# Kernel tuning notes

Hardware: AMD Instinct MI355X
Metric: run time of the kernel (lower is better)

The kernel has to match this reference:

```python
import jax, jax.numpy as jnp
import numpy as np

KNN = 4
H = 0.03


def setup_inputs() -> dict:
    key = jax.random.key(0)
    pc = jax.random.normal(key, (8, 4096, 3), dtype=jnp.float32)  # [B, N, 3]
    return {"pc": pc}


def reference(pc) -> jnp.ndarray:
    sq = jnp.sum(pc * pc, axis=-1)  # [B, N]
    # dist[b, i, j] = || pc[b,i] - pc[b,j] ||^2
    dist = sq[:, :, None] + sq[:, None, :] - 2.0 * jnp.einsum("bid,bjd->bij", pc, pc)
    dist = jnp.maximum(dist, 0.0)
    # k nearest neighbors with offset=1 (skip self): take smallest KNN+1, drop the first
    neg_top, _ = jax.lax.top_k(-dist, KNN + 1)  # sorted descending -> distances ascending
    knn_dist = -neg_top[..., 1:]  # [B, N, KNN]
    weight = jnp.exp(-knn_dist / (H * H))
    loss = jnp.sum(-knn_dist * weight)
    return loss
```

## Files before the change

### kernel.cpp

```cpp
#include <hip/hip_runtime.h>
#include <math.h>

#define NPTS   4096
#define NB     8
#define TILE   64
#define NWAVES 8
#define BLK    (NWAVES * 64)
#define JCHUNK (NPTS / NWAVES)
#define INV_H2 (1.0f / (0.03f * 0.03f))

__device__ __forceinline__ float med3f(float a, float b, float c) {
#if defined(__has_builtin)
#if __has_builtin(__builtin_amdgcn_fmed3f)
  return __builtin_amdgcn_fmed3f(a, b, c);
#else
  return fminf(c, fmaxf(a, b));
#endif
#else
  return fminf(c, fmaxf(a, b));
#endif
}

template <bool CHECK>
__device__ __forceinline__ void scan_range(const float4* __restrict__ sP,
                                           int lo, int hi, int self,
                                           float mx, float my, float mz, float sqi,
                                           float& t0, float& t1, float& t2, float& t3) {
#pragma unroll 8
  for (int j = lo; j < hi; ++j) {
    float4 q = sP[j];
    float t = fmaf(mz, q.z, q.w);
    t = fmaf(my, q.y, t);
    t = fmaf(mx, q.x, t);
    float d = t + sqi;
    if (CHECK) d = (j == self) ? 3.0e38f : d;
    t3 = med3f(t2, d, t3);
    t2 = med3f(t1, d, t2);
    t1 = med3f(t0, d, t1);
    t0 = fminf(t0, d);
  }
}

__device__ __forceinline__ void merge4(float a0, float a1, float a2, float a3,
                                       float b0, float b1, float b2, float b3,
                                       float& o0, float& o1, float& o2, float& o3) {
  float L0 = fminf(a0, b3), L1 = fminf(a1, b2), L2 = fminf(a2, b1), L3 = fminf(a3, b0);
  float e0 = fminf(L0, L2), e2 = fmaxf(L0, L2);
  float e1 = fminf(L1, L3), e3 = fmaxf(L1, L3);
  o0 = fminf(e0, e1); o1 = fmaxf(e0, e1);
  o2 = fminf(e2, e3); o3 = fmaxf(e2, e3);
}

__global__ __launch_bounds__(BLK)
void repulsion_kernel(const float* __restrict__ pc, float* __restrict__ out) {
  __shared__ float4 sP[NPTS];
  __shared__ float4 cand4[NWAVES * TILE];

  const int blk  = blockIdx.x;
  const int b    = blk >> 6;
  const int tile = blk & 63;
  const int tid  = threadIdx.x;
  const float* base = pc + (size_t)b * NPTS * 3;
  const float4* pcv = (const float4*)base;

  for (int g = tid; g < NPTS / 4; g += BLK) {
    float4 a = pcv[3 * g + 0];
    float4 c = pcv[3 * g + 1];
    float4 e = pcv[3 * g + 2];
    float x0 = a.x, y0 = a.y, z0 = a.z;
    float x1 = a.w, y1 = c.x, z1 = c.y;
    float x2 = c.z, y2 = c.w, z2 = e.x;
    float x3 = e.y, y3 = e.z, z3 = e.w;
    sP[4 * g + 0] = make_float4(x0, y0, z0, fmaf(x0, x0, fmaf(y0, y0, z0 * z0)));
    sP[4 * g + 1] = make_float4(x1, y1, z1, fmaf(x1, x1, fmaf(y1, y1, z1 * z1)));
    sP[4 * g + 2] = make_float4(x2, y2, z2, fmaf(x2, x2, fmaf(y2, y2, z2 * z2)));
    sP[4 * g + 3] = make_float4(x3, y3, z3, fmaf(x3, x3, fmaf(y3, y3, z3 * z3)));
  }
  __syncthreads();

  const int w    = tid >> 6;
  const int lane = tid & 63;
  const int self = tile * TILE + lane;

  float4 me = sP[self];
  const float mx = -2.0f * me.x, my = -2.0f * me.y, mz = -2.0f * me.z;
  const float sqi = me.w;

  const float INF = 3.0e38f;
  float t0 = INF, t1 = INF, t2 = INF, t3 = INF;

  const int j0 = w * JCHUNK;
  const int selfwave = tile >> 3;
  if (w == selfwave) {
    const int s0 = tile * TILE;
    scan_range<false>(sP, j0, s0, self, mx, my, mz, sqi, t0, t1, t2, t3);
    scan_range<true >(sP, s0, s0 + TILE, self, mx, my, mz, sqi, t0, t1, t2, t3);
    scan_range<false>(sP, s0 + TILE, j0 + JCHUNK, self, mx, my, mz, sqi, t0, t1, t2, t3);
  } else {
    scan_range<false>(sP, j0, j0 + JCHUNK, self, mx, my, mz, sqi, t0, t1, t2, t3);
  }

  cand4[w * TILE + lane] = make_float4(t0, t1, t2, t3);
  __syncthreads();

  if (tid < 64) {
    float4 A = cand4[0 * TILE + lane];
    float4 B = cand4[1 * TILE + lane];
    float4 C = cand4[2 * TILE + lane];
    float4 D = cand4[3 * TILE + lane];
    float4 E = cand4[4 * TILE + lane];
    float4 F = cand4[5 * TILE + lane];
    float4 G = cand4[6 * TILE + lane];
    float4 H4 = cand4[7 * TILE + lane];
    float ab0, ab1, ab2, ab3, cd0, cd1, cd2, cd3;
    float ef0, ef1, ef2, ef3, gh0, gh1, gh2, gh3;
    merge4(A.x, A.y, A.z, A.w, B.x, B.y, B.z, B.w, ab0, ab1, ab2, ab3);
    merge4(C.x, C.y, C.z, C.w, D.x, D.y, D.z, D.w, cd0, cd1, cd2, cd3);
    merge4(E.x, E.y, E.z, E.w, F.x, F.y, F.z, F.w, ef0, ef1, ef2, ef3);
    merge4(G.x, G.y, G.z, G.w, H4.x, H4.y, H4.z, H4.w, gh0, gh1, gh2, gh3);
    float u0, u1, u2, u3, v0, v1, v2, v3;
    merge4(ab0, ab1, ab2, ab3, cd0, cd1, cd2, cd3, u0, u1, u2, u3);
    merge4(ef0, ef1, ef2, ef3, gh0, gh1, gh2, gh3, v0, v1, v2, v3);
    float m0 = fminf(u0, v3);
    float m1 = fminf(u1, v2);
    float m2 = fminf(u2, v1);
    float m3 = fminf(u3, v0);

    float s = 0.0f;
    s -= m0 * expf(-m0 * INV_H2);
    s -= m1 * expf(-m1 * INV_H2);
    s -= m2 * expf(-m2 * INV_H2);
    s -= m3 * expf(-m3 * INV_H2);

    for (int off = 32; off > 0; off >>= 1) s += __shfl_down(s, off);
    if (lane == 0) atomicAdd(out, s);
  }
}

extern "C" void kernel_launch(void* const* d_in, const int* in_sizes, int n_in,
                              void* d_out, int out_size, void* d_ws, size_t ws_size,
                              hipStream_t stream) {
  const float* pc = (const float*)d_in[0];
  float* out = (float*)d_out;
  hipMemsetAsync(out, 0, sizeof(float), stream);
  repulsion_kernel<<<dim3(NB * (NPTS / TILE)), dim3(BLK), 0, stream>>>(pc, out);
}
```

Baseline: 82.17 us.

## Process two query points per thread and use 16 waves per block

Each thread now tracks top-4 lists for two query points, so every shared-memory load of a candidate point serves two distance computations. Blocks grow to 1024 threads (16 waves), each covering 128 query points, and the grid halves to 256 blocks. The final merge becomes a 16-way tree over 128 threads. This cuts LDS traffic per distance and the number of redundant per-block staging passes, at the cost of more registers, fewer blocks to fill the GPU, and a longer cross-wave merge.

```diff
diff --git a/kernel.cpp b/kernel.cpp
--- a/kernel.cpp
+++ b/kernel.cpp
@@ -3,11 +3,12 @@
 
 #define NPTS   4096
 #define NB     8
-#define TILE   64
-#define NWAVES 8
+#define IGRP   128
+#define NWAVES 16
 #define BLK    (NWAVES * 64)
 #define JCHUNK (NPTS / NWAVES)
 #define INV_H2 (1.0f / (0.03f * 0.03f))
+#define INFD   3.0e38f
 
 __device__ __forceinline__ float med3f(float a, float b, float c) {
 #if defined(__has_builtin)
@@ -22,109 +23,115 @@
 }
 
 template <bool CHECK>
-__device__ __forceinline__ void scan_range(const float4* __restrict__ sP,
-                                           int lo, int hi, int self,
-                                           float mx, float my, float mz, float sqi,
-                                           float& t0, float& t1, float& t2, float& t3) {
+__device__ __forceinline__ void scan_range(
+    const float4* __restrict__ sP, int lo, int hi, int i0, int i1,
+    float mx0, float my0, float mz0, float sq0,
+    float mx1, float my1, float mz1, float sq1,
+    float& a0, float& a1, float& a2, float& a3,
+    float& b0, float& b1, float& b2, float& b3) {
 #pragma unroll 8
   for (int j = lo; j < hi; ++j) {
     float4 q = sP[j];
-    float t = fmaf(mz, q.z, q.w);
-    t = fmaf(my, q.y, t);
-    t = fmaf(mx, q.x, t);
-    float d = t + sqi;
-    if (CHECK) d = (j == self) ? 3.0e38f : d;
-    t3 = med3f(t2, d, t3);
-    t2 = med3f(t1, d, t2);
-    t1 = med3f(t0, d, t1);
-    t0 = fminf(t0, d);
+    float u = fmaf(mz0, q.z, q.w);
+    u = fmaf(my0, q.y, u);
+    u = fmaf(mx0, q.x, u);
+    float d0 = u + sq0;
+    float v = fmaf(mz1, q.z, q.w);
+    v = fmaf(my1, q.y, v);
+    v = fmaf(mx1, q.x, v);
+    float d1 = v + sq1;
+    if (CHECK) {
+      d0 = (j == i0) ? INFD : d0;
+      d1 = (j == i1) ? INFD : d1;
+    }
+    a3 = med3f(a2, d0, a3); a2 = med3f(a1, d0, a2);
+    a1 = med3f(a0, d0, a1); a0 = fminf(a0, d0);
+    b3 = med3f(b2, d1, b3); b2 = med3f(b1, d1, b2);
+    b1 = med3f(b0, d1, b1); b0 = fminf(b0, d1);
   }
 }
 
-__device__ __forceinline__ void merge4(float a0, float a1, float a2, float a3,
-                                       float b0, float b1, float b2, float b3,
-                                       float& o0, float& o1, float& o2, float& o3) {
-  float L0 = fminf(a0, b3), L1 = fminf(a1, b2), L2 = fminf(a2, b1), L3 = fminf(a3, b0);
+__device__ __forceinline__ float4 merge4(float4 A, float4 B) {
+  float L0 = fminf(A.x, B.w), L1 = fminf(A.y, B.z);
+  float L2 = fminf(A.z, B.y), L3 = fminf(A.w, B.x);
   float e0 = fminf(L0, L2), e2 = fmaxf(L0, L2);
   float e1 = fminf(L1, L3), e3 = fmaxf(L1, L3);
-  o0 = fminf(e0, e1); o1 = fmaxf(e0, e1);
-  o2 = fminf(e2, e3); o3 = fmaxf(e2, e3);
+  return make_float4(fminf(e0, e1), fmaxf(e0, e1), fminf(e2, e3), fmaxf(e2, e3));
 }
 
 __global__ __launch_bounds__(BLK)
 void repulsion_kernel(const float* __restrict__ pc, float* __restrict__ out) {
   __shared__ float4 sP[NPTS];
-  __shared__ float4 cand4[NWAVES * TILE];
+  __shared__ float4 cand[NWAVES * IGRP];
 
   const int blk  = blockIdx.x;
-  const int b    = blk >> 6;
-  const int tile = blk & 63;
+  const int b    = blk >> 5;
+  const int g    = blk & 31;
   const int tid  = threadIdx.x;
-  const float* base = pc + (size_t)b * NPTS * 3;
-  const float4* pcv = (const float4*)base;
+  const float4* pcv = (const float4*)(pc + (size_t)b * NPTS * 3);
 
-  for (int g = tid; g < NPTS / 4; g += BLK) {
-    float4 a = pcv[3 * g + 0];
-    float4 c = pcv[3 * g + 1];
-    float4 e = pcv[3 * g + 2];
+  {
+    int k = tid;
+    float4 a = pcv[3 * k + 0];
+    float4 c = pcv[3 * k + 1];
+    float4 e = pcv[3 * k + 2];
     float x0 = a.x, y0 = a.y, z0 = a.z;
     float x1 = a.w, y1 = c.x, z1 = c.y;
     float x2 = c.z, y2 = c.w, z2 = e.x;
     float x3 = e.y, y3 = e.z, z3 = e.w;
-    sP[4 * g + 0] = make_float4(x0, y0, z0, fmaf(x0, x0, fmaf(y0, y0, z0 * z0)));
-    sP[4 * g + 1] = make_float4(x1, y1, z1, fmaf(x1, x1, fmaf(y1, y1, z1 * z1)));
-    sP[4 * g + 2] = make_float4(x2, y2, z2, fmaf(x2, x2, fmaf(y2, y2, z2 * z2)));
-    sP[4 * g + 3] = make_float4(x3, y3, z3, fmaf(x3, x3, fmaf(y3, y3, z3 * z3)));
+    sP[4 * k + 0] = make_float4(x0, y0, z0, fmaf(x0, x0, fmaf(y0, y0, z0 * z0)));
+    sP[4 * k + 1] = make_float4(x1, y1, z1, fmaf(x1, x1, fmaf(y1, y1, z1 * z1)));
+    sP[4 * k + 2] = make_float4(x2, y2, z2, fmaf(x2, x2, fmaf(y2, y2, z2 * z2)));
+    sP[4 * k + 3] = make_float4(x3, y3, z3, fmaf(x3, x3, fmaf(y3, y3, z3 * z3)));
   }
   __syncthreads();
 
   const int w    = tid >> 6;
   const int lane = tid & 63;
-  const int self = tile * TILE + lane;
+  const int i0   = g * IGRP + lane;
+  const int i1   = i0 + 64;
 
-  float4 me = sP[self];
-  const float mx = -2.0f * me.x, my = -2.0f * me.y, mz = -2.0f * me.z;
-  const float sqi = me.w;
+  float4 p0 = sP[i0];
+  float4 p1 = sP[i1];
+  const float mx0 = -2.0f * p0.x, my0 = -2.0f * p0.y, mz0 = -2.0f * p0.z, sq0 = p0.w;
+  const float mx1 = -2.0f * p1.x, my1 = -2.0f * p1.y, mz1 = -2.0f * p1.z, sq1 = p1.w;
 
-  const float INF = 3.0e38f;
-  float t0 = INF, t1 = INF, t2 = INF, t3 = INF;
+  float a0 = INFD, a1 = INFD, a2 = INFD, a3 = INFD;
+  float b0 = INFD, b1 = INFD, b2 = INFD, b3 = INFD;
 
   const int j0 = w * JCHUNK;
-  const int selfwave = tile >> 3;
+  const int selfwave = g >> 1;
   if (w == selfwave) {
-    const int s0 = tile * TILE;
-    scan_range<false>(sP, j0, s0, self, mx, my, mz, sqi, t0, t1, t2, t3);
-    scan_range<true >(sP, s0, s0 + TILE, self, mx, my, mz, sqi, t0, t1, t2, t3);
-    scan_range<false>(sP, s0 + TILE, j0 + JCHUNK, self, mx, my, mz, sqi, t0, t1, t2, t3);
+    const int s0 = g * IGRP;
+    scan_range<false>(sP, j0, s0, i0, i1, mx0, my0, mz0, sq0, mx1, my1, mz1, sq1,
+                      a0, a1, a2, a3, b0, b1, b2, b3);
+    scan_range<true >(sP, s0, s0 + IGRP, i0, i1, mx0, my0, mz0, sq0, mx1, my1, mz1, sq1,
+                      a0, a1, a2, a3, b0, b1, b2, b3);
+    scan_range<false>(sP, s0 + IGRP, j0 + JCHUNK, i0, i1, mx0, my0, mz0, sq0, mx1, my1, mz1, sq1,
+                      a0, a1, a2, a3, b0, b1, b2, b3);
   } else {
-    scan_range<false>(sP, j0, j0 + JCHUNK, self, mx, my, mz, sqi, t0, t1, t2, t3);
+    scan_range<false>(sP, j0, j0 + JCHUNK, i0, i1, mx0, my0, mz0, sq0, mx1, my1, mz1, sq1,
+                      a0, a1, a2, a3, b0, b1, b2, b3);
   }
 
-  cand4[w * TILE + lane] = make_float4(t0, t1, t2, t3);
+  cand[w * IGRP + lane]      = make_float4(a0, a1, a2, a3);
+  cand[w * IGRP + 64 + lane] = make_float4(b0, b1, b2, b3);
   __syncthreads();
 
-  if (tid < 64) {
-    float4 A = cand4[0 * TILE + lane];
-    float4 B = cand4[1 * TILE + lane];
-    float4 C = cand4[2 * TILE + lane];
-    float4 D = cand4[3 * TILE + lane];
-    float4 E = cand4[4 * TILE + lane];
-    float4 F = cand4[5 * TILE + lane];
-    float4 G = cand4[6 * TILE + lane];
-    float4 H4 = cand4[7 * TILE + lane];
-    float ab0, ab1, ab2, ab3, cd0, cd1, cd2, cd3;
-    float ef0, ef1, ef2, ef3, gh0, gh1, gh2, gh3;
-    merge4(A.x, A.y, A.z, A.w, B.x, B.y, B.z, B.w, ab0, ab1, ab2, ab3);
-    merge4(C.x, C.y, C.z, C.w, D.x, D.y, D.z, D.w, cd0, cd1, cd2, cd3);
-    merge4(E.x, E.y, E.z, E.w, F.x, F.y, F.z, F.w, ef0, ef1, ef2, ef3);
-    merge4(G.x, G.y, G.z, G.w, H4.x, H4.y, H4.z, H4.w, gh0, gh1, gh2, gh3);
-    float u0, u1, u2, u3, v0, v1, v2, v3;
-    merge4(ab0, ab1, ab2, ab3, cd0, cd1, cd2, cd3, u0, u1, u2, u3);
-    merge4(ef0, ef1, ef2, ef3, gh0, gh1, gh2, gh3, v0, v1, v2, v3);
-    float m0 = fminf(u0, v3);
-    float m1 = fminf(u1, v2);
-    float m2 = fminf(u2, v1);
-    float m3 = fminf(u3, v0);
+  if (tid < IGRP) {
+    float4 L[NWAVES];
+#pragma unroll
+    for (int ww = 0; ww < NWAVES; ++ww) L[ww] = cand[ww * IGRP + tid];
+#pragma unroll
+    for (int ww = 0; ww < 8; ++ww) L[ww] = merge4(L[2 * ww], L[2 * ww + 1]);
+#pragma unroll
+    for (int ww = 0; ww < 4; ++ww) L[ww] = merge4(L[2 * ww], L[2 * ww + 1]);
+    float4 U = merge4(L[0], L[1]);
+    float4 V = merge4(L[2], L[3]);
+    float m0 = fminf(U.x, V.w);
+    float m1 = fminf(U.y, V.z);
+    float m2 = fminf(U.z, V.y);
+    float m3 = fminf(U.w, V.x);
 
     float s = 0.0f;
     s -= m0 * expf(-m0 * INV_H2);
@@ -133,7 +140,7 @@
     s -= m3 * expf(-m3 * INV_H2);
 
     for (int off = 32; off > 0; off >>= 1) s += __shfl_down(s, off);
-    if (lane == 0) atomicAdd(out, s);
+    if ((tid & 63) == 0) atomicAdd(out, s);
   }
 }
 
@@ -143,5 +150,5 @@
   const float* pc = (const float*)d_in[0];
   float* out = (float*)d_out;
   hipMemsetAsync(out, 0, sizeof(float), stream);
-  repulsion_kernel<<<dim3(NB * (NPTS / TILE)), dim3(BLK), 0, stream>>>(pc, out);
+  repulsion_kernel<<<dim3(NB * (NPTS / IGRP)), dim3(BLK), 0, stream>>>(pc, out);
 }
```

New measurement: 85.23 us. 3.7% more time.
